# Kernel tuning notes

Measured on AMD Instinct MI355X. Metric: run time of the kernel, lower is better.

## Reference

```python
import jax, jax.numpy as jnp
import numpy as np

MIN_R = 0.05
MAX_R = 0.3
K = 16  # num_neighbors


def setup_inputs() -> dict:
    key = jax.random.key(0)
    k1, k2, k3 = jax.random.split(key, 3)
    B, N, M, C = 4, 16384, 2048, 64
    points = jax.random.uniform(k1, (B, N, 3), dtype=jnp.float32)
    features = jax.random.normal(k2, (B, N, C), dtype=jnp.float32)
    center_indices = jax.random.randint(k3, (B, M), 0, N)
    return {"points": points, "features": features, "center_indices": center_indices}


def reference(points, features, center_indices):
    B, N, _ = points.shape
    # gather center coordinates: [B, M, 3]
    centers = jnp.take_along_axis(points, center_indices[:, :, None], axis=1)
    # pairwise distances [B, M, N] (direct diff form, matching torch.norm)
    diff = points[:, None, :, :] - centers[:, :, None, :]
    dist = jnp.sqrt(jnp.sum(diff * diff, axis=-1))
    # density from count of points within min_radius
    init_counts = jnp.sum(dist < MIN_R, axis=-1, keepdims=True).astype(jnp.float32)
    density = init_counts / (4.0 / 3.0 * np.pi * MIN_R ** 3 + 1e-8)
    density_max = jnp.max(density) + 1e-8
    radii = MIN_R + (MAX_R - MIN_R) * (1.0 - density / density_max)  # [B, M, 1]
    # mask out points outside per-center radius, then k smallest distances
    dist = jnp.where(dist < radii, dist, 1e10)
    _, knn_indices = jax.lax.top_k(-dist, K)  # [B, M, K]
    knn_indices = jnp.clip(knn_indices, 0, N - 1)
    # gather neighbor features: [B, M, K, C]
    neighbor_features = jax.vmap(lambda f, idx: f[idx])(features, knn_indices)
    return neighbor_features
```

## Files before the change

kernel.cpp:

```cpp
#include <hip/hip_runtime.h>
#include <stdint.h>

#define BB 4
#define NN 16384
#define MM 2048
#define CC 64
#define KK 16
#define WAVES 4
#define G 16
#define NC (G * G * G)
#define SCAP 128
#define CAP 512

typedef unsigned long long u64;
typedef unsigned int u32;
typedef unsigned short u16;
typedef unsigned char u8;

__device__ __forceinline__ float axdist(float c, int cell) {
  const float lo = (float)cell * (1.0f / (float)G);
  const float hi = (float)(cell + 1) * (1.0f / (float)G);
  float d = 0.0f;
  if (c < lo) d = lo - c;
  else if (c > hi) d = c - hi;
  return d;
}

#define LGKM_WAIT() __asm__ volatile("s_waitcnt lgkmcnt(0)" ::: "memory")

__device__ __forceinline__ u64 wave_min_u64(u64 v) {
#pragma unroll
  for (int off = 32; off > 0; off >>= 1) {
    u64 o = __shfl_xor(v, off, 64);
    v = (o < v) ? o : v;
  }
  return v;
}

__global__ __launch_bounds__(256) void cell_count_kernel(
    const float* __restrict__ pts, int* __restrict__ cell_cnt) {
  const int tid = blockIdx.x * 256 + threadIdx.x;
  const int b = tid >> 14, i = tid & (NN - 1);
  const float* p = pts + (size_t)b * NN * 3 + (size_t)i * 3;
  int ix = (int)(p[0] * (float)G); ix = ix < 0 ? 0 : (ix > G - 1 ? G - 1 : ix);
  int iy = (int)(p[1] * (float)G); iy = iy < 0 ? 0 : (iy > G - 1 ? G - 1 : iy);
  int iz = (int)(p[2] * (float)G); iz = iz < 0 ? 0 : (iz > G - 1 ? G - 1 : iz);
  atomicAdd(&cell_cnt[b * NC + (iz * G + iy) * G + ix], 1);
}

__global__ __launch_bounds__(256) void cell_scan_kernel(
    const int* __restrict__ cell_cnt, int* __restrict__ cell_start) {
  __shared__ u32 wsum[WAVES];
  const int b = blockIdx.x;
  const int* cnt = cell_cnt + b * NC;
  int* st = cell_start + b * (NC + 1);
  const int base = threadIdx.x * 16;
  const int lane = threadIdx.x & 63;
  const int wave = threadIdx.x >> 6;
  int loc[16];
  int s = 0;
#pragma unroll
  for (int i = 0; i < 16; ++i) { loc[i] = s; s += cnt[base + i]; }
  u32 inc = (u32)s;
#pragma unroll
  for (int off = 1; off < 64; off <<= 1) {
    u32 t = __shfl_up(inc, off, 64);
    if (lane >= off) inc += t;
  }
  if (lane == 63) wsum[wave] = inc;
  __syncthreads();
  u32 woff = 0;
#pragma unroll
  for (int w = 0; w < WAVES; ++w) woff += (w < wave) ? wsum[w] : 0u;
  const u32 off = woff + inc - (u32)s;
#pragma unroll
  for (int i = 0; i < 16; ++i) st[base + i] = (int)(off + (u32)loc[i]);
  if (threadIdx.x == 0) st[NC] = NN;
}

__global__ __launch_bounds__(256) void cell_fill_kernel(
    const float* __restrict__ pts, const int* __restrict__ cell_start,
    int* __restrict__ cursor, float4* __restrict__ sorted) {
  const int tid = blockIdx.x * 256 + threadIdx.x;
  const int b = tid >> 14, i = tid & (NN - 1);
  const float* p = pts + (size_t)b * NN * 3 + (size_t)i * 3;
  const float x = p[0], y = p[1], z = p[2];
  int ix = (int)(x * (float)G); ix = ix < 0 ? 0 : (ix > G - 1 ? G - 1 : ix);
  int iy = (int)(y * (float)G); iy = iy < 0 ? 0 : (iy > G - 1 ? G - 1 : iy);
  int iz = (int)(z * (float)G); iz = iz < 0 ? 0 : (iz > G - 1 ? G - 1 : iz);
  const int cell = (iz * G + iy) * G + ix;
  const int pos = cell_start[b * (NC + 1) + cell] + atomicAdd(&cursor[b * NC + cell], 1);
  sorted[(size_t)b * NN + pos] = make_float4(x, y, z, __uint_as_float((u32)i));
}

__global__ __launch_bounds__(256) void grid_count_kernel(
    const float* __restrict__ points, const int* __restrict__ cidx,
    const int* __restrict__ cell_start, const float4* __restrict__ sorted,
    int* __restrict__ counts, int* __restrict__ maxcnt) {
#pragma clang fp contract(off)
  const int sub = threadIdx.x & 15;
  const int grp = threadIdx.x >> 4;
  const int center = blockIdx.x * 16 + grp;
  const int b = center >> 11;
  const float* pb = points + (size_t)b * (NN * 3);
  const int ci = cidx[center];
  const float ccx = pb[ci * 3 + 0], ccy = pb[ci * 3 + 1], ccz = pb[ci * 3 + 2];
  const float R0 = 0.05f;
  const float rc = R0 * 1.0001f + 1e-6f;
  const float rc2 = rc * rc;
  const int lox = max(0, (int)floorf((ccx - rc) * (float)G));
  const int hix = min(G - 1, (int)floorf((ccx + rc) * (float)G));
  const int loy = max(0, (int)floorf((ccy - rc) * (float)G));
  const int hiy = min(G - 1, (int)floorf((ccy + rc) * (float)G));
  const int loz = max(0, (int)floorf((ccz - rc) * (float)G));
  const int hiz = min(G - 1, (int)floorf((ccz + rc) * (float)G));
  const int cs0 = b * (NC + 1);
  const float4* sp = sorted + (size_t)b * NN;
  int cnt = 0;
  for (int zc = loz; zc <= hiz; ++zc) {
    const float dz0 = axdist(ccz, zc);
    for (int yc = loy; yc <= hiy; ++yc) {
      const float dy0 = axdist(ccy, yc);
      const float dd = dy0 * dy0 + dz0 * dz0;
      if (dd >= rc2) continue;
      const float half = sqrtf(rc2 - dd) * 1.0001f + 1e-6f;
      const int xl = max(lox, (int)floorf((ccx - half) * (float)G));
      const int xh = min(hix, (int)floorf((ccx + half) * (float)G));
      if (xl > xh) continue;
      const int row = cs0 + (zc * G + yc) * G;
      const int s0 = cell_start[row + xl];
      const int e0 = cell_start[row + xh + 1];
      for (int p = s0 + sub; p < e0; p += 16) {
        const float4 pt = sp[p];
        const float dx = pt.x - ccx, dy = pt.y - ccy, dz = pt.z - ccz;
        const float d = sqrtf((dx * dx + dy * dy) + dz * dz);
        cnt += (d < R0) ? 1 : 0;
      }
    }
  }
#pragma unroll
  for (int off = 8; off > 0; off >>= 1) cnt += __shfl_xor(cnt, off, 16);
  if (sub == 0) {
    counts[center] = cnt;
    atomicMax(maxcnt, cnt);
  }
}

#define WALK(BODY)                                                   \
  {                                                                  \
    int ri = 0;                                                      \
    for (u32 w = (u32)lane; w < T; w += 64) {                        \
      while (rowC[ri + 1] <= w) ++ri;                                \
      const int p = (int)rowS[ri] + (int)(w - rowC[ri]);             \
      const float4 pt = sp[p];                                       \
      const float dx = pt.x - ccx, dy = pt.y - ccy, dz = pt.z - ccz; \
      const float d = sqrtf((dx * dx + dy * dy) + dz * dz);          \
      BODY                                                           \
    }                                                                \
  }

__global__ __launch_bounds__(256, 6) void grid_topk_kernel(
    const float* __restrict__ points, const float* __restrict__ features,
    const int* __restrict__ cidx, const int* __restrict__ counts,
    const int* __restrict__ maxcnt, const int* __restrict__ cell_start,
    const float4* __restrict__ sorted, float* __restrict__ out) {
#pragma clang fp contract(off)
  __shared__ u16 cand_s[WAVES][CAP];
  __shared__ u8  candb_s[WAVES][CAP];
  __shared__ u64 surv_s[WAVES][SCAP + 2];
  __shared__ u32 rowS_s[WAVES][128];
  __shared__ u32 rowC_s[WAVES][128];
  __shared__ u32 hist_s[WAVES][128];

  const int lane = threadIdx.x & 63;
  const int wave = threadIdx.x >> 6;
  const int center = blockIdx.x * WAVES + wave;
  const int b = center >> 11;
  u16* cand = cand_s[wave];
  u8*  candb = candb_s[wave];
  u64* surv = surv_s[wave];
  u32* rowS = rowS_s[wave];
  u32* rowC = rowC_s[wave];
  u32* hist = hist_s[wave];
  const u64 lanemask = (((u64)1 << lane) - 1);

  const float* pb = points + (size_t)b * (NN * 3);
  const int ci = cidx[center];
  const float ccx = pb[ci * 3 + 0], ccy = pb[ci * 3 + 1], ccz = pb[ci * 3 + 2];

  const int cnt_c = counts[center];
  const float DENOM = (float)(4.0 / 3.0 * 3.141592653589793 * (0.05 * 0.05 * 0.05) + 1e-8);
  const float dens = (float)cnt_c / DENOM;
  const float dmax = (float)(*maxcnt) / DENOM + 1e-8f;
  const float r = 0.05f + 0.25f * (1.0f - dens / dmax);
  const int cs0 = b * (NC + 1);
  const float4* sp = sorted + (size_t)b * NN;

  const float tA = fminf(r, fmaxf(0.055f,
      0.05f * cbrtf(16.0f / fmaxf((float)cnt_c, 0.5f)) * 1.35f));

  u32 scnt = 0;

  for (int attempt = 0; attempt < 2; ++attempt) {
    const float t_eff = (attempt == 0) ? tA : r;
    const bool finals = (attempt == 1) || (tA >= r);
    const float rc = t_eff * 1.0001f + 1e-6f;
    const float rc2 = rc * rc;
    const float bs1 = 32.0f / t_eff;
    const float bs2 = 1024.0f / t_eff;

    const int lox = max(0, (int)floorf((ccx - rc) * (float)G));
    const int hix = min(G - 1, (int)floorf((ccx + rc) * (float)G));
    const int loy = max(0, (int)floorf((ccy - rc) * (float)G));
    const int hiy = min(G - 1, (int)floorf((ccy + rc) * (float)G));
    const int loz = max(0, (int)floorf((ccz - rc) * (float)G));
    const int hiz = min(G - 1, (int)floorf((ccz + rc) * (float)G));

    const int ny = hiy - loy + 1;
    const int nrows = ny * (hiz - loz + 1);
    u32 len0 = 0, len1 = 0, st0 = 0, st1 = 0;
#pragma unroll
    for (int half_i = 0; half_i < 2; ++half_i) {
      const int rr = lane + half_i * 64;
      u32 st = 0, len = 0;
      if (rr < nrows) {
        const int zz = rr / ny, yy = rr - zz * ny;
        const int zc = loz + zz, yc = loy + yy;
        const float dz0 = axdist(ccz, zc);
        const float dy0 = axdist(ccy, yc);
        const float dd = dy0 * dy0 + dz0 * dz0;
        if (dd < rc2) {
          const float half = sqrtf(rc2 - dd) * 1.0001f + 1e-6f;
          const int xl = max(lox, (int)floorf((ccx - half) * (float)G));
          const int xh = min(hix, (int)floorf((ccx + half) * (float)G));
          if (xl <= xh) {
            const int row = cs0 + (zc * G + yc) * G;
            const int s0 = cell_start[row + xl];
            const int e0 = cell_start[row + xh + 1];
            st = (u32)s0; len = (u32)(e0 - s0);
          }
        }
      }
      if (half_i == 0) { st0 = st; len0 = len; } else { st1 = st; len1 = len; }
    }
    u32 a = len0;
#pragma unroll
    for (int off = 1; off < 64; off <<= 1) {
      u32 t = __shfl_up(a, off, 64);
      if (lane >= off) a += t;
    }
    const u32 tot0 = __shfl(a, 63, 64);
    u32 bcum = len1;
#pragma unroll
    for (int off = 1; off < 64; off <<= 1) {
      u32 t = __shfl_up(bcum, off, 64);
      if (lane >= off) bcum += t;
    }
    const u32 T = tot0 + __shfl(bcum, 63, 64);
    rowS[lane] = st0;
    rowS[lane + 64] = st1;
    rowC[lane] = a - len0;
    rowC[lane + 64] = tot0 + bcum - len1;
    hist[lane] = 0;
    hist[lane + 64] = 0;
    LGKM_WAIT();

    u32 scn = 0;
    {
      int riA = 0, riB = 0;
      for (u32 w = (u32)lane; w < T; w += 128) {
        while (rowC[riA + 1] <= w) ++riA;
        const int pA = (int)rowS[riA] + (int)(w - rowC[riA]);
        const float4 ptA = sp[pA];
        const u32 w2 = w + 64;
        const bool hasB = (w2 < T);
        int pB = 0;
        float xB = 4e4f, yB = 4e4f, zB = 4e4f;
        if (hasB) {
          if (riB < riA) riB = riA;
          while (rowC[riB + 1] <= w2) ++riB;
          pB = (int)rowS[riB] + (int)(w2 - rowC[riB]);
          const float4 ptB = sp[pB];
          xB = ptB.x; yB = ptB.y; zB = ptB.z;
        }
        const float dxA = ptA.x - ccx, dyA = ptA.y - ccy, dzA = ptA.z - ccz;
        const float dA = sqrtf((dxA * dxA + dyA * dyA) + dzA * dzA);
        const float dxB = xB - ccx, dyB = yB - ccy, dzB = zB - ccz;
        const float dB = sqrtf((dxB * dxB + dyB * dyB) + dzB * dzB);
        const bool accA = dA < t_eff;
        const bool accB = hasB && (dB < t_eff);
        const u64 maskA = __ballot(accA);
        const u64 maskB = __ballot(accB);
        if (accA) {
          int bin = (int)(dA * bs1); bin = bin > 31 ? 31 : bin;
          atomicAdd(&hist[((lane & 3) << 5) + bin], 1u);
          const u32 pos = scn + (u32)__popcll(maskA & lanemask);
          if (pos < (u32)CAP) { cand[pos] = (u16)pA; candb[pos] = (u8)bin; }
        }
        const u32 cA = (u32)__popcll(maskA);
        if (accB) {
          int bin = (int)(dB * bs1); bin = bin > 31 ? 31 : bin;
          atomicAdd(&hist[((lane & 3) << 5) + bin], 1u);
          const u32 pos = scn + cA + (u32)__popcll(maskB & lanemask);
          if (pos < (u32)CAP) { cand[pos] = (u16)pB; candb[pos] = (u8)bin; }
        }
        scn += cA + (u32)__popcll(maskB);
      }
    }
    LGKM_WAIT();

    u32 incl = 0;
    if (lane < 32) incl = hist[lane] + hist[lane + 32] + hist[lane + 64] + hist[lane + 96];
#pragma unroll
    for (int off = 1; off < 32; off <<= 1) {
      u32 t = __shfl_up(incl, off, 32);
      if ((lane & 31) >= off) incl += t;
    }
    const u32 total = __shfl(incl, 31, 64);
    const bool overflow = total > (u32)CAP;

    if (total < (u32)KK) {
      if (!finals) continue;
      for (u32 i = lane; i < total; i += 64) {
        const float4 pt = sp[cand[i]];
        const float dx = pt.x - ccx, dy = pt.y - ccy, dz = pt.z - ccz;
        const float d = sqrtf((dx * dx + dy * dy) + dz * dz);
        surv[i] = ((u64)__float_as_uint(d) << 32) | __float_as_uint(pt.w);
      }
      scnt = total;
      LGKM_WAIT();
      break;
    }

    u64 bm = __ballot(lane < 32 && incl >= (u32)KK);
    const int b1 = (__ffsll(bm) - 1);
    const u32 cnt_b1 = __shfl(incl, b1, 64);
    const u32 pre = (b1 > 0) ? __shfl(incl, b1 - 1, 64) : 0u;

    int b2 = 31;
    const bool need2 = (pre + cnt_b1 > (u32)SCAP);
    if (need2) {
      hist[lane] = 0;
      hist[lane + 64] = 0;
      LGKM_WAIT();
      if (!overflow) {
        for (u32 i = lane; i < total; i += 64) {
          if ((int)candb[i] == b1) {
            const float4 pt = sp[cand[i]];
            const float dx = pt.x - ccx, dy = pt.y - ccy, dz = pt.z - ccz;
            const float d = sqrtf((dx * dx + dy * dy) + dz * dz);
            int o = (int)(d * bs2) - (b1 << 5);
            o = o < 0 ? 0 : (o > 31 ? 31 : o);
            atomicAdd(&hist[((lane & 3) << 5) + o], 1u);
          }
        }
      } else {
        WALK({
          if (d < t_eff) {
            int bin = (int)(d * bs1); bin = bin > 31 ? 31 : bin;
            if (bin == b1) {
              int o = (int)(d * bs2) - (b1 << 5);
              o = o < 0 ? 0 : (o > 31 ? 31 : o);
              atomicAdd(&hist[((lane & 3) << 5) + o], 1u);
            }
          }
        })
      }
      LGKM_WAIT();
      u32 incl2 = 0;
      if (lane < 32) incl2 = hist[lane] + hist[lane + 32] + hist[lane + 64] + hist[lane + 96];
#pragma unroll
      for (int off = 1; off < 32; off <<= 1) {
        u32 t = __shfl_up(incl2, off, 32);
        if ((lane & 31) >= off) incl2 += t;
      }
      const u32 target = (u32)KK - pre;
      u64 bm2 = __ballot(lane < 32 && incl2 >= target);
      b2 = bm2 ? (__ffsll(bm2) - 1) : 31;
    }

    u32 sc = 0;
    if (!overflow) {
      for (u32 i = lane; i < total; i += 64) {
        const int bin = (int)candb[i];
        bool acc2;
        float d = 0.0f;
        u32 pw = 0;
        if (!need2) {
          acc2 = (bin <= b1);
          if (acc2) {
            const float4 pt = sp[cand[i]];
            const float dx = pt.x - ccx, dy = pt.y - ccy, dz = pt.z - ccz;
            d = sqrtf((dx * dx + dy * dy) + dz * dz);
            pw = __float_as_uint(pt.w);
          }
        } else {
          acc2 = (bin < b1);
          if (bin == b1) {
            const float4 pt = sp[cand[i]];
            const float dx = pt.x - ccx, dy = pt.y - ccy, dz = pt.z - ccz;
            d = sqrtf((dx * dx + dy * dy) + dz * dz);
            pw = __float_as_uint(pt.w);
            int o = (int)(d * bs2) - (b1 << 5);
            o = o < 0 ? 0 : (o > 31 ? 31 : o);
            acc2 = (o <= b2);
          } else if (acc2) {
            const float4 pt = sp[cand[i]];
            const float dx = pt.x - ccx, dy = pt.y - ccy, dz = pt.z - ccz;
            d = sqrtf((dx * dx + dy * dy) + dz * dz);
            pw = __float_as_uint(pt.w);
          }
        }
        const u64 mask = __ballot(acc2);
        if (acc2) {
          const u32 pos = sc + (u32)__popcll(mask & lanemask);
          if (pos < (u32)SCAP)
            surv[pos] = ((u64)__float_as_uint(d) << 32) | pw;
        }
        sc += (u32)__popcll(mask);
      }
    } else {
      WALK({
        bool acc2 = false;
        if (d < t_eff) {
          int bin = (int)(d * bs1); bin = bin > 31 ? 31 : bin;
          if (!need2) acc2 = (bin <= b1);
          else {
            int o = (int)(d * bs2) - (b1 << 5);
            o = o < 0 ? 0 : (o > 31 ? 31 : o);
            acc2 = (bin < b1) || (bin == b1 && o <= b2);
          }
        }
        const u64 mask = __ballot(acc2);
        if (acc2) {
          const u32 pos = sc + (u32)__popcll(mask & lanemask);
          if (pos < (u32)SCAP)
            surv[pos] = ((u64)__float_as_uint(d) << 32) | __float_as_uint(pt.w);
        }
        sc += (u32)__popcll(mask);
      })
    }
    sc = (u32)__shfl((int)sc, 0, 64);
    scnt = sc > (u32)SCAP ? (u32)SCAP : sc;
    LGKM_WAIT();
    break;
  }

  if (scnt < (u32)KK) {
    for (int base = 0; base < NN && scnt < (u32)KK; base += 64) {
      const int i = base + lane;
      const float x = pb[i * 3 + 0], y = pb[i * 3 + 1], z = pb[i * 3 + 2];
      const float dx = x - ccx, dy = y - ccy, dz = z - ccz;
      const float d = sqrtf((dx * dx + dy * dy) + dz * dz);
      u64 m = __ballot(!(d < r));
      while (m && scnt < (u32)KK) {
        const int t = __ffsll(m) - 1;
        m &= m - 1;
        if (lane == 0)
          surv[scnt] = ((u64)__float_as_uint(1e10f) << 32) | (u32)(base + t);
        scnt++;
      }
    }
    LGKM_WAIT();
  }

  {
    const u64 k0 = (lane < (int)scnt) ? surv[lane] : ~0ULL;
    const u64 k1 = (lane + 64 < (int)scnt) ? surv[lane + 64] : ~0ULL;
    u32 rank0 = 0, rank1 = 0;
    for (u32 j = 0; j < scnt; ++j) {
      const u64 kj = surv[j];
      rank0 += (kj < k0) ? 1u : 0u;
      rank1 += (kj < k1) ? 1u : 0u;
    }
    if (lane < (int)scnt && rank0 < (u32)KK) rowS[rank0] = (u32)(k0 & 0xffffffffULL);
    if (lane + 64 < (int)scnt && rank1 < (u32)KK) rowS[rank1] = (u32)(k1 & 0xffffffffULL);
    LGKM_WAIT();
  }

  const float* fb = features + (size_t)b * NN * CC;
  float* ob = out + (size_t)center * KK * CC;
  const int ch4 = (lane & 15) * 4;
  const int ksub = lane >> 4;
#pragma unroll
  for (int kq = 0; kq < 4; ++kq) {
    const int k = kq * 4 + ksub;
    const int nk = (int)rowS[k];
    const float4 v = *(const float4*)(fb + (size_t)nk * CC + ch4);
    *(float4*)(ob + (size_t)k * CC + ch4) = v;
  }
}

#define CH 4096
#define NCHUNK (NN / CH)

__global__ __launch_bounds__(256) void fb_count_kernel(
    const float* __restrict__ points, const int* __restrict__ cidx,
    int* __restrict__ counts, int* __restrict__ maxcnt) {
#pragma clang fp contract(off)
  __shared__ float s[CH * 3];
  const int lane = threadIdx.x & 63;
  const int wave = threadIdx.x >> 6;
  const int center = blockIdx.x * WAVES + wave;
  const int b = center >> 11;
  const float* pb = points + (size_t)b * (NN * 3);
  const int ci = cidx[center];
  const float cx = pb[ci * 3 + 0], cy = pb[ci * 3 + 1], cz = pb[ci * 3 + 2];
  int cnt = 0;
  for (int c = 0; c < NCHUNK; ++c) {
    __syncthreads();
    const float4* src = (const float4*)(pb + (size_t)c * CH * 3);
    float4* dst = (float4*)s;
    for (int i = threadIdx.x; i < CH * 3 / 4; i += 256) dst[i] = src[i];
    __syncthreads();
    for (int j = 0; j < CH / 64; ++j) {
      const int p = j * 64 + lane;
      const float dx = s[p * 3 + 0] - cx;
      const float dy = s[p * 3 + 1] - cy;
      const float dz = s[p * 3 + 2] - cz;
      const float d = sqrtf((dx * dx + dy * dy) + dz * dz);
      cnt += (d < 0.05f) ? 1 : 0;
    }
  }
#pragma unroll
  for (int off = 32; off > 0; off >>= 1) cnt += __shfl_xor(cnt, off, 64);
  if (lane == 0) { counts[center] = cnt; atomicMax(maxcnt, cnt); }
}

__global__ __launch_bounds__(256) void fb_topk_kernel(
    const float* __restrict__ points, const float* __restrict__ features,
    const int* __restrict__ cidx, const int* __restrict__ counts,
    const int* __restrict__ maxcnt, float* __restrict__ out) {
#pragma clang fp contract(off)
  __shared__ float s[CH * 3];
  const int lane = threadIdx.x & 63;
  const int wave = threadIdx.x >> 6;
  const int center = blockIdx.x * WAVES + wave;
  const int b = center >> 11;
  const float* pb = points + (size_t)b * (NN * 3);
  const int ci = cidx[center];
  const float cx = pb[ci * 3 + 0], cy = pb[ci * 3 + 1], cz = pb[ci * 3 + 2];
  const float DENOM = (float)(4.0 / 3.0 * 3.141592653589793 * (0.05 * 0.05 * 0.05) + 1e-8);
  const float dens = (float)counts[center] / DENOM;
  const float dmax = (float)(*maxcnt) / DENOM + 1e-8f;
  const float r = 0.05f + 0.25f * (1.0f - dens / dmax);
  u64 kb[KK];
#pragma unroll
  for (int i = 0; i < KK; ++i) kb[i] = ~0ULL;
  u64 worst = ~0ULL, T = ~0ULL;
  for (int c = 0; c < NCHUNK; ++c) {
    __syncthreads();
    const float4* src = (const float4*)(pb + (size_t)c * CH * 3);
    float4* dst = (float4*)s;
    for (int i = threadIdx.x; i < CH * 3 / 4; i += 256) dst[i] = src[i];
    __syncthreads();
    const int nbase = c * CH;
    for (int j = 0; j < CH / 64; ++j) {
      const int p = j * 64 + lane;
      const float dx = s[p * 3 + 0] - cx;
      const float dy = s[p * 3 + 1] - cy;
      const float dz = s[p * 3 + 2] - cz;
      const float d = sqrtf((dx * dx + dy * dy) + dz * dz);
      const float dm = (d < r) ? d : 1e10f;
      const u64 key = ((u64)__float_as_uint(dm) << 32) | (unsigned)(nbase + p);
      if (key < T && key < worst) {
        u64 cc = key;
#pragma unroll
        for (int i = 0; i < KK; ++i) {
          const bool lt = kb[i] < cc;
          const u64 lo = lt ? kb[i] : cc;
          const u64 hi = lt ? cc : kb[i];
          kb[i] = lo; cc = hi;
        }
        worst = kb[KK - 1];
      }
    }
    if (c == 0) {
      u64 t[KK];
#pragma unroll
      for (int i = 0; i < KK; ++i) t[i] = kb[i];
      u64 g = 0;
#pragma unroll
      for (int k = 0; k < KK; ++k) {
        g = wave_min_u64(t[0]);
        if (t[0] == g) {
#pragma unroll
          for (int i = 0; i < KK - 1; ++i) t[i] = t[i + 1];
          t[KK - 1] = ~0ULL;
        }
      }
      T = g;
    }
  }
  int knn[KK];
#pragma unroll
  for (int k = 0; k < KK; ++k) {
    const u64 g = wave_min_u64(kb[0]);
    if (kb[0] == g) {
#pragma unroll
      for (int i = 0; i < KK - 1; ++i) kb[i] = kb[i + 1];
      kb[KK - 1] = ~0ULL;
    }
    knn[k] = (int)(unsigned)(g & 0xffffffffULL);
  }
  const float* fb = features + (size_t)b * NN * CC;
  float* ob = out + (size_t)center * KK * CC;
#pragma unroll
  for (int k = 0; k < KK; ++k) ob[k * CC + lane] = fb[(size_t)knn[k] * CC + lane];
}

extern "C" void kernel_launch(void* const* d_in, const int* in_sizes, int n_in,
                              void* d_out, int out_size, void* d_ws, size_t ws_size,
                              hipStream_t stream) {
  const float* points   = (const float*)d_in[0];
  const float* features = (const float*)d_in[1];
  const int*   cidx     = (const int*)d_in[2];
  float* out = (float*)d_out;

  char* w = (char*)d_ws;
  const size_t off_cellcnt = 16;
  const size_t off_cursor  = off_cellcnt + (size_t)BB * NC * 4;
  const size_t zero_bytes  = off_cursor + (size_t)BB * NC * 4;
  const size_t off_counts  = zero_bytes;
  const size_t off_cstart  = off_counts + (size_t)BB * MM * 4;
  const size_t off_sorted  = (off_cstart + (size_t)BB * (NC + 1) * 4 + 15) & ~(size_t)15;
  const size_t need        = off_sorted + (size_t)BB * NN * 16;

  int* maxcnt = (int*)w;
  dim3 block(256);

  if (ws_size >= need) {
    int* cell_cnt   = (int*)(w + off_cellcnt);
    int* cursor     = (int*)(w + off_cursor);
    int* counts     = (int*)(w + off_counts);
    int* cell_start = (int*)(w + off_cstart);
    float4* sorted  = (float4*)(w + off_sorted);

    hipMemsetAsync(w, 0, zero_bytes, stream);
    cell_count_kernel<<<dim3(BB * NN / 256), block, 0, stream>>>(points, cell_cnt);
    cell_scan_kernel<<<dim3(BB), block, 0, stream>>>(cell_cnt, cell_start);
    cell_fill_kernel<<<dim3(BB * NN / 256), block, 0, stream>>>(points, cell_start, cursor, sorted);
    grid_count_kernel<<<dim3(BB * MM / 16), block, 0, stream>>>(
        points, cidx, cell_start, sorted, counts, maxcnt);
    grid_topk_kernel<<<dim3(BB * MM / WAVES), block, 0, stream>>>(
        points, features, cidx, counts, maxcnt, cell_start, sorted, out);
  } else {
    int* counts = (int*)w + 16;
    hipMemsetAsync(maxcnt, 0, sizeof(int), stream);
    fb_count_kernel<<<dim3(BB * MM / WAVES), block, 0, stream>>>(points, cidx, counts, maxcnt);
    fb_topk_kernel<<<dim3(BB * MM / WAVES), block, 0, stream>>>(points, features, cidx, counts, maxcnt, out);
  }
}
```

Measured before the change: 70.35 us.

## Fuse grid build into one per-batch kernel with shared-memory counting sort

Replaces the memset plus three build kernels (count, scan, fill) with one 1024-thread block per batch that builds the cell histogram in LDS, scans it, and scatters points into sorted order using LDS atomics. It also resets maxcnt inside that kernel and makes grid_count reduce its maximum per block before a single global atomicMax. The aim is to cut launch overhead and global atomics. The trade-off is that only 4 blocks run the build, so it uses very little of the GPU's parallelism.

```diff
diff --git a/kernel.cpp b/kernel.cpp
--- a/kernel.cpp
+++ b/kernel.cpp
@@ -37,60 +37,70 @@
   return v;
 }
 
-__global__ __launch_bounds__(256) void cell_count_kernel(
-    const float* __restrict__ pts, int* __restrict__ cell_cnt) {
-  const int tid = blockIdx.x * 256 + threadIdx.x;
-  const int b = tid >> 14, i = tid & (NN - 1);
-  const float* p = pts + (size_t)b * NN * 3 + (size_t)i * 3;
-  int ix = (int)(p[0] * (float)G); ix = ix < 0 ? 0 : (ix > G - 1 ? G - 1 : ix);
-  int iy = (int)(p[1] * (float)G); iy = iy < 0 ? 0 : (iy > G - 1 ? G - 1 : iy);
-  int iz = (int)(p[2] * (float)G); iz = iz < 0 ? 0 : (iz > G - 1 ? G - 1 : iz);
-  atomicAdd(&cell_cnt[b * NC + (iz * G + iy) * G + ix], 1);
-}
-
-__global__ __launch_bounds__(256) void cell_scan_kernel(
-    const int* __restrict__ cell_cnt, int* __restrict__ cell_start) {
-  __shared__ u32 wsum[WAVES];
+__global__ __launch_bounds__(1024) void build4_kernel(
+    const float* __restrict__ pts, int* __restrict__ cell_start,
+    float4* __restrict__ sorted, int* __restrict__ maxcnt) {
+  __shared__ int hist[NC];
+  __shared__ int wsum[16];
   const int b = blockIdx.x;
-  const int* cnt = cell_cnt + b * NC;
-  int* st = cell_start + b * (NC + 1);
-  const int base = threadIdx.x * 16;
-  const int lane = threadIdx.x & 63;
-  const int wave = threadIdx.x >> 6;
-  int loc[16];
-  int s = 0;
-#pragma unroll
-  for (int i = 0; i < 16; ++i) { loc[i] = s; s += cnt[base + i]; }
-  u32 inc = (u32)s;
+  const int t = threadIdx.x;
+  const int lane = t & 63;
+  const int wave = t >> 6;
+
+  if (b == 0 && t == 0) *maxcnt = 0;
+
+  for (int i = t; i < NC; i += 1024) hist[i] = 0;
+  __syncthreads();
+
+  const float* pb = pts + (size_t)b * NN * 3;
+  int mycell[16];
+#pragma unroll
+  for (int j = 0; j < 16; ++j) {
+    const int i = t + j * 1024;
+    const float x = pb[i * 3 + 0], y = pb[i * 3 + 1], z = pb[i * 3 + 2];
+    int ix = (int)(x * (float)G); ix = ix < 0 ? 0 : (ix > G - 1 ? G - 1 : ix);
+    int iy = (int)(y * (float)G); iy = iy < 0 ? 0 : (iy > G - 1 ? G - 1 : iy);
+    int iz = (int)(z * (float)G); iz = iz < 0 ? 0 : (iz > G - 1 ? G - 1 : iz);
+    const int cell = (iz * G + iy) * G + ix;
+    mycell[j] = cell;
+    atomicAdd(&hist[cell], 1);
+  }
+  __syncthreads();
+
+  const int base = t * 4;
+  const int l0 = hist[base], l1 = hist[base + 1], l2 = hist[base + 2], l3 = hist[base + 3];
+  const int s4 = l0 + l1 + l2 + l3;
+  u32 inc = (u32)s4;
 #pragma unroll
   for (int off = 1; off < 64; off <<= 1) {
-    u32 t = __shfl_up(inc, off, 64);
-    if (lane >= off) inc += t;
-  }
-  if (lane == 63) wsum[wave] = inc;
+    u32 tt = __shfl_up(inc, off, 64);
+    if (lane >= off) inc += tt;
+  }
+  if (lane == 63) wsum[wave] = (int)inc;
   __syncthreads();
   u32 woff = 0;
-#pragma unroll
-  for (int w = 0; w < WAVES; ++w) woff += (w < wave) ? wsum[w] : 0u;
-  const u32 off = woff + inc - (u32)s;
-#pragma unroll
-  for (int i = 0; i < 16; ++i) st[base + i] = (int)(off + (u32)loc[i]);
-  if (threadIdx.x == 0) st[NC] = NN;
-}
-
-__global__ __launch_bounds__(256) void cell_fill_kernel(
-    const float* __restrict__ pts, const int* __restrict__ cell_start,
-    int* __restrict__ cursor, float4* __restrict__ sorted) {
-  const int tid = blockIdx.x * 256 + threadIdx.x;
-  const int b = tid >> 14, i = tid & (NN - 1);
-  const float* p = pts + (size_t)b * NN * 3 + (size_t)i * 3;
-  const float x = p[0], y = p[1], z = p[2];
-  int ix = (int)(x * (float)G); ix = ix < 0 ? 0 : (ix > G - 1 ? G - 1 : ix);
-  int iy = (int)(y * (float)G); iy = iy < 0 ? 0 : (iy > G - 1 ? G - 1 : iy);
-  int iz = (int)(z * (float)G); iz = iz < 0 ? 0 : (iz > G - 1 ? G - 1 : iz);
-  const int cell = (iz * G + iy) * G + ix;
-  const int pos = cell_start[b * (NC + 1) + cell] + atomicAdd(&cursor[b * NC + cell], 1);
-  sorted[(size_t)b * NN + pos] = make_float4(x, y, z, __uint_as_float((u32)i));
+  for (int w2 = 0; w2 < wave; ++w2) woff += (u32)wsum[w2];
+  const int ex = (int)(woff + inc - (u32)s4);
+  hist[base] = ex;
+  hist[base + 1] = ex + l0;
+  hist[base + 2] = ex + l0 + l1;
+  hist[base + 3] = ex + l0 + l1 + l2;
+  int* st = cell_start + b * (NC + 1);
+  st[base] = ex;
+  st[base + 1] = ex + l0;
+  st[base + 2] = ex + l0 + l1;
+  st[base + 3] = ex + l0 + l1 + l2;
+  if (t == 0) st[NC] = NN;
+  __syncthreads();
+
+  float4* sp = sorted + (size_t)b * NN;
+#pragma unroll
+  for (int j = 0; j < 16; ++j) {
+    const int i = t + j * 1024;
+    const float x = pb[i * 3 + 0], y = pb[i * 3 + 1], z = pb[i * 3 + 2];
+    const int pos = atomicAdd(&hist[mycell[j]], 1);
+    sp[pos] = make_float4(x, y, z, __uint_as_float((u32)i));
+  }
 }
 
 __global__ __launch_bounds__(256) void grid_count_kernel(
@@ -98,10 +108,13 @@
     const int* __restrict__ cell_start, const float4* __restrict__ sorted,
     int* __restrict__ counts, int* __restrict__ maxcnt) {
 #pragma clang fp contract(off)
+  __shared__ int bmax;
   const int sub = threadIdx.x & 15;
   const int grp = threadIdx.x >> 4;
   const int center = blockIdx.x * 16 + grp;
   const int b = center >> 11;
+  if (threadIdx.x == 0) bmax = 0;
+  __syncthreads();
   const float* pb = points + (size_t)b * (NN * 3);
   const int ci = cidx[center];
   const float ccx = pb[ci * 3 + 0], ccy = pb[ci * 3 + 1], ccz = pb[ci * 3 + 2];
@@ -142,8 +155,10 @@
   for (int off = 8; off > 0; off >>= 1) cnt += __shfl_xor(cnt, off, 16);
   if (sub == 0) {
     counts[center] = cnt;
-    atomicMax(maxcnt, cnt);
-  }
+    atomicMax(&bmax, cnt);
+  }
+  __syncthreads();
+  if (threadIdx.x == 0) atomicMax(maxcnt, bmax);
 }
 
 #define WALK(BODY)                                                   \
@@ -618,10 +633,7 @@
   float* out = (float*)d_out;
 
   char* w = (char*)d_ws;
-  const size_t off_cellcnt = 16;
-  const size_t off_cursor  = off_cellcnt + (size_t)BB * NC * 4;
-  const size_t zero_bytes  = off_cursor + (size_t)BB * NC * 4;
-  const size_t off_counts  = zero_bytes;
+  const size_t off_counts  = 256;
   const size_t off_cstart  = off_counts + (size_t)BB * MM * 4;
   const size_t off_sorted  = (off_cstart + (size_t)BB * (NC + 1) * 4 + 15) & ~(size_t)15;
   const size_t need        = off_sorted + (size_t)BB * NN * 16;
@@ -630,22 +642,17 @@
   dim3 block(256);
 
   if (ws_size >= need) {
-    int* cell_cnt   = (int*)(w + off_cellcnt);
-    int* cursor     = (int*)(w + off_cursor);
     int* counts     = (int*)(w + off_counts);
     int* cell_start = (int*)(w + off_cstart);
     float4* sorted  = (float4*)(w + off_sorted);
 
-    hipMemsetAsync(w, 0, zero_bytes, stream);
-    cell_count_kernel<<<dim3(BB * NN / 256), block, 0, stream>>>(points, cell_cnt);
-    cell_scan_kernel<<<dim3(BB), block, 0, stream>>>(cell_cnt, cell_start);
-    cell_fill_kernel<<<dim3(BB * NN / 256), block, 0, stream>>>(points, cell_start, cursor, sorted);
+    build4_kernel<<<dim3(BB), dim3(1024), 0, stream>>>(points, cell_start, sorted, maxcnt);
     grid_count_kernel<<<dim3(BB * MM / 16), block, 0, stream>>>(
         points, cidx, cell_start, sorted, counts, maxcnt);
     grid_topk_kernel<<<dim3(BB * MM / WAVES), block, 0, stream>>>(
         points, features, cidx, counts, maxcnt, cell_start, sorted, out);
   } else {
-    int* counts = (int*)w + 16;
+    int* counts = (int*)w + 64;
     hipMemsetAsync(maxcnt, 0, sizeof(int), stream);
     fb_count_kernel<<<dim3(BB * MM / WAVES), block, 0, stream>>>(points, cidx, counts, maxcnt);
     fb_topk_kernel<<<dim3(BB * MM / WAVES), block, 0, stream>>>(points, features, cidx, counts, maxcnt, out);
```

After: 58.48 us (median of 2 runs). -16.9%, faster.
